# Performance work log

Hardware: AMD Instinct MI355X
Metric: run time of the kernel (lower is better)

## Reference

```python
import jax, jax.numpy as jnp
import numpy as np

B, C, H, W = 16, 256, 64, 64
P, HEADS, D = 8, 8, 32  # window size, heads, channels per head


def setup_inputs() -> dict:
    key = jax.random.key(0)
    k1, k2, k3, k4 = jax.random.split(key, 4)
    x = jax.random.normal(k1, (B, C, H, W), jnp.float32)
    # kaiming-ish init for the 1x1 convs (stored as [out, in] matrices)
    w_proj = jax.random.normal(k2, (3 * HEADS * D, C), jnp.float32) * (2.0 / C) ** 0.5
    # original inits position to zeros; use small noise so the bias path is exercised
    position = jax.random.normal(k3, (HEADS, 2 * P, 2 * P), jnp.float32) * 0.02
    w_out = jax.random.normal(k4, (C, HEADS * D), jnp.float32) * (2.0 / (HEADS * D)) ** 0.5
    b_out = jnp.zeros((C,), jnp.float32)
    return {"x": x, "w_proj": w_proj, "position": position, "w_out": w_out, "b_out": b_out}


def _rel_bias(position):
    # unfolded_posenc: relative offsets between all pairs of positions in a PxP window
    coords = jnp.stack(jnp.meshgrid(jnp.arange(P), jnp.arange(P), indexing="ij"), -1).reshape(P * P, 2)
    rel = coords[None, :, :] - coords[:, None, :] + P  # [P^2, P^2, 2], values in [1, 2P-1]
    return position[:, rel[..., 0], rel[..., 1]]  # [heads, P^2, P^2]


def reference(x, w_proj, position, w_out, b_out):
    b, c, h, w = x.shape
    nh, nw = h // P, w // P
    # 1x1 conv projection to qkv: [B, 3*heads*D, H, W]
    qkv = jnp.einsum("bchw,oc->bohw", x, w_proj)
    # window partition -> [3, B, heads, nh, nw, P*P, D]
    qkv = qkv.reshape(b, 3, HEADS, D, nh, P, nw, P)
    qkv = qkv.transpose(1, 0, 2, 4, 6, 5, 7, 3).reshape(3, b, HEADS, nh, nw, P * P, D)
    q, k, v = qkv[0], qkv[1], qkv[2]
    bias = _rel_bias(position)  # [heads, P^2, P^2]
    scale = 1.0 / jnp.sqrt(jnp.asarray(D, x.dtype))
    scores = jnp.einsum("bhnmqd,bhnmkd->bhnmqk", q, k) * scale + bias[None, :, None, None]
    attn = jax.nn.softmax(scores, axis=-1)
    o = jnp.einsum("bhnmqk,bhnmkd->bhnmqd", attn, v)  # [B, heads, nh, nw, P^2, D]
    # fold windows back to [B, heads*D, H, W]
    o = o.reshape(b, HEADS, nh, nw, P, P, D)
    o = o.transpose(0, 1, 6, 2, 4, 3, 5).reshape(b, HEADS * D, h, w)
    # output 1x1 conv with bias
    return jnp.einsum("bchw,oc->bohw", o, w_out) + b_out[None, :, None, None]
```

## Files before the change

kernel.cpp:

```cpp
#include <hip/hip_runtime.h>


typedef _Float16 f16x8 __attribute__((ext_vector_type(8)));
typedef _Float16 f16x4v __attribute__((ext_vector_type(4)));
typedef float    f32x4 __attribute__((ext_vector_type(4)));
typedef unsigned short u16;
typedef unsigned int   u32;
typedef unsigned long long u64;

#define SCALE 0.17677669529663687f
#define QK_S  40
#define VT_S  72
#define PB_S  40
#define LT_S  264
#define XW_S  264
#define OT_S  264

__device__ __forceinline__ u16 f2hu(float f) {
    _Float16 h = (_Float16)f; return __builtin_bit_cast(u16, h);
}
__device__ __forceinline__ u64 pack4h(f32x4 v) {
    u32 lo = __builtin_bit_cast(u32, __builtin_amdgcn_cvt_pkrtz(v[0], v[1]));
    u32 hi = __builtin_bit_cast(u32, __builtin_amdgcn_cvt_pkrtz(v[2], v[3]));
    return ((u64)hi << 32) | (u64)lo;
}
__device__ __forceinline__ f16x8 cat44(f16x4v a, f16x4v b) {
    return __builtin_shufflevector(a, b, 0, 1, 2, 3, 4, 5, 6, 7);
}

__global__ __launch_bounds__(512)
void prep(const float* __restrict__ x, const float* __restrict__ wp,
          const float* __restrict__ wo, u16* __restrict__ xtw,
          u16* __restrict__ w16k, u16* __restrict__ wo16k)
{
    __shared__ u16 Lt[64 * LT_S];
    const int bid = blockIdx.x;
    const int tid = threadIdx.x;
    if (bid < 1024) {
        const int y = bid & 63, b = bid >> 6;
        const int yq = y >> 3, py = y & 7;
        const float* xb = x + ((size_t)b * 256) * 4096 + y * 64;
        #pragma unroll
        for (int i = 0; i < 8; ++i) {
            int idx = tid + i * 512;
            int c = idx >> 4, w4 = (idx & 15) << 2;
            float4 v = *(const float4*)(xb + (size_t)c * 4096 + w4);
            float vv[4] = {v.x, v.y, v.z, v.w};
            #pragma unroll
            for (int j = 0; j < 4; ++j) {
                int w = w4 + j;
                Lt[w * LT_S + (c ^ (((w >> 2) & 7) << 3))] = f2hu(vv[j]);
            }
        }
        __syncthreads();
        u16* dst = xtw + (size_t)(b * 64 + yq * 8) * 16384;
        #pragma unroll
        for (int i = 0; i < 4; ++i) {
            int idx = tid + i * 512;
            int w = idx >> 5, c8 = (idx & 31) << 3;
            f16x8 v = *(const f16x8*)(&Lt[w * LT_S + (c8 ^ (((w >> 2) & 7) << 3))]);
            *(f16x8*)(dst + (w >> 3) * 16384 + (py * 8 + (w & 7)) * 256 + c8) = v;
        }
    } else {
        int idx = (bid - 1024) * 512 + tid;
        if (idx < 196608) {
            int hq = idx / 98304, o = idx - hq * 98304;
            int kt = o / 12288, o2 = o - kt * 12288;
            int lr = o2 >> 5, cc = o2 & 31;
            int s = lr >> 7, hh = (lr >> 5) & 3, d = lr & 31;
            w16k[idx] = f2hu(wp[(size_t)(s * 256 + (hq * 4 + hh) * 32 + d) * 256 + kt * 32 + cc]);
        } else {
            int j = idx - 196608;
            int kt = j >> 13, o2 = j & 8191;
            int row = o2 >> 5, cc = o2 & 31;
            wo16k[j] = f2hu(wo[(size_t)row * 256 + kt * 32 + cc]);
        }
    }
}

__global__ __launch_bounds__(512, 4)
void lsa_qkv_attn_xt(const u16* __restrict__ xtw, const u16* __restrict__ w16k,
                     const float* __restrict__ position, u16* __restrict__ Ows)
{
    __shared__ u16 U[29696];
    __shared__ float POSL[1024];
    u16* XwL = U;
    u16* Qb  = U;
    u16* Kb  = U + 10240;
    u16* Vt  = U + 20480;

    const int tid = threadIdx.x;
    const int hq = blockIdx.x & 1, win = blockIdx.x >> 1, b = blockIdx.y;
    const int w = tid >> 6, m = tid & 15, lg = (tid >> 4) & 3;

    *(float2*)(&POSL[tid * 2]) = *(const float2*)(position + hq * 1024 + tid * 2);
    {
        const u16* xwin = xtw + (size_t)(b * 64 + win) * 16384;
        #pragma unroll
        for (int i = 0; i < 4; ++i) {
            int g = tid + i * 512;
            *(f16x8*)(XwL + (g >> 5) * XW_S + (g & 31) * 8) = *(const f16x8*)(xwin + g * 8);
        }
    }
    __syncthreads();

    f32x4 acc[3][4];
    int isv[3], hhv[3], d0v[3], lr0v[3];
    {
        const f32x4 z = {0.f, 0.f, 0.f, 0.f};
        #pragma unroll
        for (int i = 0; i < 3; ++i) {
            #pragma unroll
            for (int nt = 0; nt < 4; ++nt) acc[i][nt] = z;
            int lr0 = (3 * w + i) * 16;
            lr0v[i] = lr0;
            isv[i] = lr0 >> 7; hhv[i] = (lr0 >> 5) & 3; d0v[i] = lr0 & 31;
        }
        const u16* wbase = w16k + (size_t)hq * 98304;
        #pragma unroll
        for (int kt = 0; kt < 8; ++kt) {
            f16x8 af[3], bf[4];
            #pragma unroll
            for (int i = 0; i < 3; ++i)
                af[i] = *(const f16x8*)(wbase + kt * 12288 + (lr0v[i] + m) * 32 + lg * 8);
            #pragma unroll
            for (int nt = 0; nt < 4; ++nt)
                bf[nt] = *(const f16x8*)(XwL + (nt * 16 + m) * XW_S + kt * 32 + lg * 8);
            #pragma unroll
            for (int i = 0; i < 3; ++i)
                #pragma unroll
                for (int nt = 0; nt < 4; ++nt)
                    acc[i][nt] = __builtin_amdgcn_mfma_f32_16x16x32_f16(af[i], bf[nt], acc[i][nt], 0, 0, 0);
        }
    }
    __syncthreads();

    {
        #pragma unroll
        for (int i = 0; i < 3; ++i) {
            int i_s = isv[i], hh = hhv[i], d0 = d0v[i];
            #pragma unroll
            for (int nt = 0; nt < 4; ++nt) {
                int pix = nt * 16 + m;
                if (i_s < 2) {
                    u16* base = (i_s == 0) ? Qb : Kb;
                    *(u64*)(base + hh * 64 * QK_S + pix * QK_S + d0 + lg * 4) = pack4h(acc[i][nt]);
                } else {
                    #pragma unroll
                    for (int r = 0; r < 4; ++r)
                        Vt[hh * 32 * VT_S + (d0 + lg * 4 + r) * VT_S + pix] = f2hu(acc[i][nt][r]);
                }
            }
        }
    }
    __syncthreads();

    {
        const int hh = w >> 1, qh = w & 1;
        const u16* Qh = Qb + hh * 64 * QK_S;
        const u16* Kh = Kb + hh * 64 * QK_S;
        const u16* Vh = Vt + hh * 32 * VT_S;
        const float* posh = &POSL[hh * 256];

        f16x8 kf[4], qf[2];
        #pragma unroll
        for (int kt = 0; kt < 4; ++kt)
            kf[kt] = *(const f16x8*)(Kh + (kt * 16 + m) * QK_S + lg * 8);
        #pragma unroll
        for (int qi = 0; qi < 2; ++qi)
            qf[qi] = *(const f16x8*)(Qh + ((2 * qh + qi) * 16 + m) * QK_S + lg * 8);

        const f32x4 z = {0.f, 0.f, 0.f, 0.f};
        f32x4 st[4][2];
        #pragma unroll
        for (int kt = 0; kt < 4; ++kt)
            #pragma unroll
            for (int qi = 0; qi < 2; ++qi)
                st[kt][qi] = __builtin_amdgcn_mfma_f32_16x16x32_f16(kf[kt], qf[qi], z, 0, 0, 0);

        float inv[2];
        #pragma unroll
        for (int qi = 0; qi < 2; ++qi) {
            int q = (2 * qh + qi) * 16 + m, qy = q >> 3, qx = q & 7;
            float mx = -1e30f;
            #pragma unroll
            for (int kt = 0; kt < 4; ++kt)
                #pragma unroll
                for (int r = 0; r < 4; ++r) {
                    int k = kt * 16 + lg * 4 + r, ky = k >> 3, kx = k & 7;
                    float t = st[kt][qi][r] * SCALE + posh[(ky - qy + 8) * 16 + (kx - qx + 8)];
                    st[kt][qi][r] = t;
                    mx = fmaxf(mx, t);
                }
            mx = fmaxf(mx, __shfl_xor(mx, 16));
            mx = fmaxf(mx, __shfl_xor(mx, 32));
            float sum = 0.f;
            #pragma unroll
            for (int kt = 0; kt < 4; ++kt)
                #pragma unroll
                for (int r = 0; r < 4; ++r) {
                    float e = __expf(st[kt][qi][r] - mx);
                    st[kt][qi][r] = e; sum += e;
                }
            sum += __shfl_xor(sum, 16);
            sum += __shfl_xor(sum, 32);
            inv[qi] = 1.f / sum;
        }

        f32x4 ot[2][2];
        ot[0][0] = z; ot[0][1] = z; ot[1][0] = z; ot[1][1] = z;
        #pragma unroll
        for (int ks = 0; ks < 2; ++ks) {
            f16x8 pf[2], vf[2];
            #pragma unroll
            for (int qi = 0; qi < 2; ++qi) {
                f16x4v lo = __builtin_bit_cast(f16x4v, pack4h(st[2 * ks + 0][qi] * inv[qi]));
                f16x4v hi = __builtin_bit_cast(f16x4v, pack4h(st[2 * ks + 1][qi] * inv[qi]));
                pf[qi] = cat44(lo, hi);
            }
            #pragma unroll
            for (int dt = 0; dt < 2; ++dt) {
                const u16* vrow = Vh + (dt * 16 + m) * VT_S + lg * 4;
                f16x4v v0 = *(const f16x4v*)(vrow + (2 * ks + 0) * 16);
                f16x4v v1 = *(const f16x4v*)(vrow + (2 * ks + 1) * 16);
                vf[dt] = cat44(v0, v1);
            }
            #pragma unroll
            for (int qi = 0; qi < 2; ++qi)
                #pragma unroll
                for (int dt = 0; dt < 2; ++dt)
                    ot[qi][dt] = __builtin_amdgcn_mfma_f32_16x16x32_f16(pf[qi], vf[dt], ot[qi][dt], 0, 0, 0);
        }

        const size_t obase = (size_t)(b * 64 + win) * 16384;
        const int head = hq * 4 + hh;
        #pragma unroll
        for (int qi = 0; qi < 2; ++qi)
            #pragma unroll
            for (int dt = 0; dt < 2; ++dt) {
                int c = head * 32 + dt * 16 + m;
                #pragma unroll
                for (int r = 0; r < 4; ++r) {
                    int q = (2 * qh + qi) * 16 + lg * 4 + r;
                    Ows[obase + q * 256 + c] = f2hu(ot[qi][dt][r]);
                }
            }
    }
}

__global__ __launch_bounds__(512, 4)
void lsa_outproj_row(const u16* __restrict__ Ows, const u16* __restrict__ wo16k,
                     const float* __restrict__ b_out, float* __restrict__ out)
{
    __shared__ u16 Ot[64 * OT_S];

    const int tid = threadIdx.x;
    const int y = blockIdx.x, b = blockIdx.y;
    const int yq = y >> 3, py = y & 7;
    const int w = tid >> 6, m = tid & 15, lg = (tid >> 4) & 3;

    {
        const u16* slab = Ows + (size_t)(b * 64 + yq * 8) * 16384 + (py * 8) * 256;
        #pragma unroll
        for (int i = 0; i < 4; ++i) {
            int g = tid + i * 512;
            int wx = g >> 8, gg = g & 255;
            int lx = gg >> 5, c8 = (gg & 31) << 3;
            f16x8 v = *(const f16x8*)(slab + (size_t)wx * 16384 + lx * 256 + c8);
            *(f16x8*)(Ot + (wx * 8 + lx) * OT_S + c8) = v;
        }
    }
    __syncthreads();

    f32x4 oa[2][4];
    {
        const f32x4 z = {0.f, 0.f, 0.f, 0.f};
        #pragma unroll
        for (int mt = 0; mt < 2; ++mt)
            #pragma unroll
            for (int nt = 0; nt < 4; ++nt) oa[mt][nt] = z;
    }
    #pragma unroll
    for (int kt = 0; kt < 8; ++kt) {
        f16x8 wf[2], of[4];
        #pragma unroll
        for (int mt = 0; mt < 2; ++mt)
            wf[mt] = *(const f16x8*)(wo16k + kt * 8192 + (w * 32 + mt * 16 + m) * 32 + lg * 8);
        #pragma unroll
        for (int nt = 0; nt < 4; ++nt)
            of[nt] = *(const f16x8*)(Ot + (nt * 16 + m) * OT_S + kt * 32 + lg * 8);
        #pragma unroll
        for (int mt = 0; mt < 2; ++mt)
            #pragma unroll
            for (int nt = 0; nt < 4; ++nt)
                oa[mt][nt] = __builtin_amdgcn_mfma_f32_16x16x32_f16(wf[mt], of[nt], oa[mt][nt], 0, 0, 0);
    }
    float* ob = out + (size_t)b * 1048576 + y * 64;
    #pragma unroll
    for (int mt = 0; mt < 2; ++mt)
        #pragma unroll
        for (int nt = 0; nt < 4; ++nt) {
            int px = nt * 16 + m;
            #pragma unroll
            for (int r = 0; r < 4; ++r) {
                int oc = w * 32 + mt * 16 + lg * 4 + r;
                ob[(size_t)oc * 4096 + px] = oa[mt][nt][r] + b_out[oc];
            }
        }
}

extern "C" void kernel_launch(void* const* d_in, const int* in_sizes, int n_in,
                              void* d_out, int out_size, void* d_ws, size_t ws_size,
                              hipStream_t stream) {
    const float* x      = (const float*)d_in[0];
    const float* w_proj = (const float*)d_in[1];
    const float* pos    = (const float*)d_in[2];
    const float* w_out  = (const float*)d_in[3];
    const float* b_out  = (const float*)d_in[4];
    float* out = (float*)d_out;

    u16* xtw   = (u16*)d_ws;
    u16* w16k  = (u16*)((char*)d_ws + 33554432);
    u16* wo16k = (u16*)((char*)d_ws + 33554432 + 393216);
    u16* Ows   = (u16*)((char*)d_ws + 33554432 + 393216 + 131072);

    prep<<<1536, 512, 0, stream>>>(x, w_proj, w_out, xtw, w16k, wo16k);
    lsa_qkv_attn_xt<<<dim3(128, 16), 512, 0, stream>>>(xtw, w16k, pos, Ows);
    lsa_outproj_row<<<dim3(64, 16), 512, 0, stream>>>(Ows, wo16k, b_out, out);
}
```

Measured before the change: 88.60 us.

## Keep Q projection in registers and shrink LDS to raise occupancy

Each wave now computes the Q tile it needs for attention directly and feeds the MFMA accumulators into the QK^T operand in registers, instead of writing Q to shared memory and reading it back. K is read with a matching permuted d-ordering so the dot product stays consistent. This removes the Q buffer from LDS (shrinking U) and raises the launch-bounds occupancy target from 4 to 6 blocks. The risks are register pressure under the tighter occupancy bound, and some redundant weight loads because Q rows are now loaded per head pair rather than split evenly across waves.

```diff
diff --git a/kernel.cpp b/kernel.cpp
--- a/kernel.cpp
+++ b/kernel.cpp
@@ -11,7 +11,6 @@
 #define SCALE 0.17677669529663687f
 #define QK_S  40
 #define VT_S  72
-#define PB_S  40
 #define LT_S  264
 #define XW_S  264
 #define OT_S  264
@@ -78,20 +77,20 @@
     }
 }
 
-__global__ __launch_bounds__(512, 4)
+__global__ __launch_bounds__(512, 6)
 void lsa_qkv_attn_xt(const u16* __restrict__ xtw, const u16* __restrict__ w16k,
                      const float* __restrict__ position, u16* __restrict__ Ows)
 {
-    __shared__ u16 U[29696];
+    __shared__ u16 U[19456];
     __shared__ float POSL[1024];
     u16* XwL = U;
-    u16* Qb  = U;
-    u16* Kb  = U + 10240;
-    u16* Vt  = U + 20480;
+    u16* Kb  = U;
+    u16* Vt  = U + 10240;
 
     const int tid = threadIdx.x;
     const int hq = blockIdx.x & 1, win = blockIdx.x >> 1, b = blockIdx.y;
     const int w = tid >> 6, m = tid & 15, lg = (tid >> 4) & 3;
+    const int hh = w >> 1, qh = w & 1;
 
     *(float2*)(&POSL[tid * 2]) = *(const float2*)(position + hq * 1024 + tid * 2);
     {
@@ -104,51 +103,63 @@
     }
     __syncthreads();
 
-    f32x4 acc[3][4];
-    int isv[3], hhv[3], d0v[3], lr0v[3];
+    f32x4 accQ[2][2];
+    f32x4 accKV[2][4];
+    int lrowKV[2], isvKV[2], hhKV[2], d0KV[2];
     {
         const f32x4 z = {0.f, 0.f, 0.f, 0.f};
         #pragma unroll
-        for (int i = 0; i < 3; ++i) {
-            #pragma unroll
-            for (int nt = 0; nt < 4; ++nt) acc[i][nt] = z;
-            int lr0 = (3 * w + i) * 16;
-            lr0v[i] = lr0;
-            isv[i] = lr0 >> 7; hhv[i] = (lr0 >> 5) & 3; d0v[i] = lr0 & 31;
+        for (int t = 0; t < 2; ++t) { accQ[t][0] = z; accQ[t][1] = z; }
+        #pragma unroll
+        for (int j = 0; j < 2; ++j) {
+            #pragma unroll
+            for (int nt = 0; nt < 4; ++nt) accKV[j][nt] = z;
+            int t2 = 2 * w + j;
+            isvKV[j] = t2 >> 3;
+            hhKV[j] = (t2 >> 1) & 3;
+            d0KV[j] = (t2 & 1) * 16;
+            lrowKV[j] = (1 + isvKV[j]) * 128 + hhKV[j] * 32 + d0KV[j];
         }
         const u16* wbase = w16k + (size_t)hq * 98304;
         #pragma unroll
         for (int kt = 0; kt < 8; ++kt) {
-            f16x8 af[3], bf[4];
-            #pragma unroll
-            for (int i = 0; i < 3; ++i)
-                af[i] = *(const f16x8*)(wbase + kt * 12288 + (lr0v[i] + m) * 32 + lg * 8);
+            f16x8 afq[2], afkv[2], bf[4];
+            #pragma unroll
+            for (int t = 0; t < 2; ++t)
+                afq[t] = *(const f16x8*)(wbase + kt * 12288 + (hh * 32 + t * 16 + m) * 32 + lg * 8);
+            #pragma unroll
+            for (int j = 0; j < 2; ++j)
+                afkv[j] = *(const f16x8*)(wbase + kt * 12288 + (lrowKV[j] + m) * 32 + lg * 8);
             #pragma unroll
             for (int nt = 0; nt < 4; ++nt)
                 bf[nt] = *(const f16x8*)(XwL + (nt * 16 + m) * XW_S + kt * 32 + lg * 8);
             #pragma unroll
-            for (int i = 0; i < 3; ++i)
+            for (int t = 0; t < 2; ++t)
+                #pragma unroll
+                for (int n = 0; n < 2; ++n)
+                    accQ[t][n] = __builtin_amdgcn_mfma_f32_16x16x32_f16(afq[t], bf[2 * qh + n], accQ[t][n], 0, 0, 0);
+            #pragma unroll
+            for (int j = 0; j < 2; ++j)
                 #pragma unroll
                 for (int nt = 0; nt < 4; ++nt)
-                    acc[i][nt] = __builtin_amdgcn_mfma_f32_16x16x32_f16(af[i], bf[nt], acc[i][nt], 0, 0, 0);
+                    accKV[j][nt] = __builtin_amdgcn_mfma_f32_16x16x32_f16(afkv[j], bf[nt], accKV[j][nt], 0, 0, 0);
         }
     }
     __syncthreads();
 
     {
         #pragma unroll
-        for (int i = 0; i < 3; ++i) {
-            int i_s = isv[i], hh = hhv[i], d0 = d0v[i];
+        for (int j = 0; j < 2; ++j) {
+            int hhj = hhKV[j], d0j = d0KV[j];
             #pragma unroll
             for (int nt = 0; nt < 4; ++nt) {
                 int pix = nt * 16 + m;
-                if (i_s < 2) {
-                    u16* base = (i_s == 0) ? Qb : Kb;
-                    *(u64*)(base + hh * 64 * QK_S + pix * QK_S + d0 + lg * 4) = pack4h(acc[i][nt]);
+                if (isvKV[j] == 0) {
+                    *(u64*)(Kb + hhj * 64 * QK_S + pix * QK_S + d0j + lg * 4) = pack4h(accKV[j][nt]);
                 } else {
                     #pragma unroll
                     for (int r = 0; r < 4; ++r)
-                        Vt[hh * 32 * VT_S + (d0 + lg * 4 + r) * VT_S + pix] = f2hu(acc[i][nt][r]);
+                        Vt[hhj * 32 * VT_S + (d0j + lg * 4 + r) * VT_S + pix] = f2hu(accKV[j][nt][r]);
                 }
             }
         }
@@ -156,19 +167,25 @@
     __syncthreads();
 
     {
-        const int hh = w >> 1, qh = w & 1;
-        const u16* Qh = Qb + hh * 64 * QK_S;
         const u16* Kh = Kb + hh * 64 * QK_S;
         const u16* Vh = Vt + hh * 32 * VT_S;
         const float* posh = &POSL[hh * 256];
 
-        f16x8 kf[4], qf[2];
-        #pragma unroll
-        for (int kt = 0; kt < 4; ++kt)
-            kf[kt] = *(const f16x8*)(Kh + (kt * 16 + m) * QK_S + lg * 8);
-        #pragma unroll
-        for (int qi = 0; qi < 2; ++qi)
-            qf[qi] = *(const f16x8*)(Qh + ((2 * qh + qi) * 16 + m) * QK_S + lg * 8);
+        f16x8 qf[2];
+        #pragma unroll
+        for (int qi = 0; qi < 2; ++qi) {
+            f16x4v q0 = __builtin_bit_cast(f16x4v, pack4h(accQ[0][qi]));
+            f16x4v q1 = __builtin_bit_cast(f16x4v, pack4h(accQ[1][qi]));
+            qf[qi] = cat44(q0, q1);
+        }
+        f16x8 kf[4];
+        #pragma unroll
+        for (int kt = 0; kt < 4; ++kt) {
+            const u16* krow = Kh + (kt * 16 + m) * QK_S + lg * 4;
+            f16x4v k0 = *(const f16x4v*)(krow);
+            f16x4v k1 = *(const f16x4v*)(krow + 16);
+            kf[kt] = cat44(k0, k1);
+        }
 
         const f32x4 z = {0.f, 0.f, 0.f, 0.f};
         f32x4 st[4][2];
```

Result: slower. 275.1 us (+210.5%).
